# Optimization experiments

Measured on AMD Instinct MI355X. Metric: run time of the kernel, lower is better.

The kernel has to match this reference:

```python
import jax, jax.numpy as jnp
import numpy as np

EMB_DIM = 768
NUM_HEADS = 12
OUT_DIM = 768


def setup_inputs() -> dict:
    key = jax.random.key(0)
    k_x, k_q, k_k, k_v, k_o = jax.random.split(key, 5)
    B, N, D = 8, 1024, EMB_DIM
    s = 1.0 / np.sqrt(D)
    return {
        "x": jax.random.normal(k_x, (B, N, D), dtype=jnp.float32),
        # torch nn.Linear weights are stored [out_features, in_features]
        "Wq": jax.random.normal(k_q, (D, D), dtype=jnp.float32) * s,
        "Wk": jax.random.normal(k_k, (D, D), dtype=jnp.float32) * s,
        "Wv": jax.random.normal(k_v, (D, D), dtype=jnp.float32) * s,
        "Wo": jax.random.normal(k_o, (OUT_DIM, D), dtype=jnp.float32) * s,
    }


def _split_heads(t, H):
    # [B, N, D] -> [B*H, N, D//H]  (heads folded into batch, per einsum 'b i d')
    B, N, D = t.shape
    return t.reshape(B, N, H, D // H).transpose(0, 2, 1, 3).reshape(B * H, N, D // H)


def _merge_heads(t, B, H):
    BH, N, dh = t.shape
    return t.reshape(B, H, N, dh).transpose(0, 2, 1, 3).reshape(B, N, H * dh)


def reference(x, Wq, Wk, Wv, Wo):
    B, N, D = x.shape
    H = NUM_HEADS
    dh = D // H
    # q/k/v projections (torch Linear: y = x @ W.T, no bias)
    q = _split_heads(x @ Wq.T, H)
    k = _split_heads(x @ Wk.T, H)
    v = _split_heads(x @ Wv.T, H)
    scale = dh ** (-0.5)
    # dots: 'b i d , b j d -> b i j' -> full [B*H, N, N] score matrix
    dots = jnp.einsum('bid,bjd->bij', q, k) * scale
    attn = jax.nn.softmax(dots, axis=-1)
    # dropout p=0.0 -> identity
    # vect: 'b i d , b d j -> b i j' == attn @ v
    vect = jnp.einsum('bij,bjd->bid', attn, v)
    out = _merge_heads(vect, B, H) @ Wo.T
    return out
```

## Files before the change

kernel.cpp:

```cpp
#include <hip/hip_runtime.h>
#include <hip/hip_bf16.h>
#include <stdint.h>


typedef __bf16 bf16x8 __attribute__((ext_vector_type(8)));
typedef __bf16 bf16x4 __attribute__((ext_vector_type(4)));
typedef float f32x4 __attribute__((ext_vector_type(4)));

#define GAS __attribute__((address_space(1)))
#define LAS __attribute__((address_space(3)))

__device__ __forceinline__ void glds16(const short* gp, short* lp) {
  __builtin_amdgcn_global_load_lds((const GAS void*)gp, (LAS void*)lp, 16, 0, 0);
}

__device__ __forceinline__ float fast_exp2(float x) {
#if __has_builtin(__builtin_amdgcn_exp2f)
  return __builtin_amdgcn_exp2f(x);
#else
  return __expf(x * 0.6931471805599453f);
#endif
}

__device__ __forceinline__ short bfbits(float f) {
  __bf16 b = (__bf16)f;
  union { __bf16 b; short s; } cv; cv.b = b;
  return cv.s;
}

__device__ __forceinline__ void stage8_f32(const float* __restrict__ src, short* dst) {
  float4 f0 = ((const float4*)src)[0];
  float4 f1 = ((const float4*)src)[1];
  bf16x8 t;
  t[0] = (__bf16)f0.x; t[1] = (__bf16)f0.y; t[2] = (__bf16)f0.z; t[3] = (__bf16)f0.w;
  t[4] = (__bf16)f1.x; t[5] = (__bf16)f1.y; t[6] = (__bf16)f1.z; t[7] = (__bf16)f1.w;
  *(bf16x8*)dst = t;
}

__global__ __launch_bounds__(256) void convert_kernel(
    const float* __restrict__ x, const float* __restrict__ Wq,
    const float* __restrict__ Wk, const float* __restrict__ Wv,
    short* __restrict__ xb, short* __restrict__ wqkv) {
  int seg = blockIdx.y;
  const float* src; short* dst; int n8;
  if (seg == 0) { src = x; dst = xb; n8 = 786432; }
  else {
    src = (seg == 1) ? Wq : (seg == 2) ? Wk : Wv;
    dst = wqkv + (size_t)(seg - 1) * 589824;
    n8 = 73728;
  }
  int idx = blockIdx.x * 256 + threadIdx.x;
  if (idx >= n8) return;
  stage8_f32(src + (size_t)idx * 8, dst + (size_t)idx * 8);
}

__global__ __launch_bounds__(256) void gemm_qkv(
    const short* __restrict__ xb, const short* __restrict__ wqkv,
    short* __restrict__ q, short* __restrict__ k, short* __restrict__ vt) {
  const int m0 = blockIdx.x * 128;
  const int by = blockIdx.y;
  const int n0g = by * 128;
  const int tid = threadIdx.x;
  const int w = tid >> 6, lane = tid & 63, l16 = lane & 15, quad = lane >> 4;
  const int wr = w >> 1, wc = w & 1;

  __shared__ short sA[128 * 64];
  __shared__ short sB[128 * 64];

  f32x4 acc[4][4];
#pragma unroll
  for (int i = 0; i < 4; ++i)
#pragma unroll
    for (int j = 0; j < 4; ++j) acc[i][j] = (f32x4){0.f, 0.f, 0.f, 0.f};

  for (int k0 = 0; k0 < 768; k0 += 64) {
    __syncthreads();
    const short* Ab = xb + (size_t)m0 * 768 + k0;
    const short* Bb = wqkv + (size_t)n0g * 768 + k0;
#pragma unroll
    for (int p = 0; p < 4; ++p) {
      int lin = (w * 4 + p) * 64 + lane;
      int row = lin >> 3;
      int cs = ((lin & 7) ^ (row & 7)) * 8;
      glds16(Ab + (size_t)row * 768 + cs, &sA[lin * 8]);
      glds16(Bb + (size_t)row * 768 + cs, &sB[lin * 8]);
    }
    __syncthreads();
#pragma unroll
    for (int kk2 = 0; kk2 < 2; ++kk2) {
      bf16x8 af[4], bfg[4];
#pragma unroll
      for (int t = 0; t < 4; ++t) {
        int ra = wr * 64 + t * 16 + l16;
        af[t] = *(const bf16x8*)&sA[ra * 64 + (((kk2 * 4 + quad) ^ (ra & 7)) << 3)];
        int rb = wc * 64 + t * 16 + l16;
        bfg[t] = *(const bf16x8*)&sB[rb * 64 + (((kk2 * 4 + quad) ^ (rb & 7)) << 3)];
      }
#pragma unroll
      for (int ti = 0; ti < 4; ++ti)
#pragma unroll
        for (int tj = 0; tj < 4; ++tj)
          acc[ti][tj] = __builtin_amdgcn_mfma_f32_16x16x32_bf16(af[ti], bfg[tj], acc[ti][tj], 0, 0, 0);
    }
  }

  const int wsel = by / 6;
  const int nl0 = (by % 6) * 128 + wc * 64;
  if (wsel == 2) {
#pragma unroll
    for (int ti = 0; ti < 4; ++ti)
#pragma unroll
      for (int tj = 0; tj < 4; ++tj) {
        int token = m0 + wr * 64 + ti * 16 + quad * 4;
        int nl = nl0 + tj * 16 + l16;
        int bh = (token >> 10) * 12 + (nl >> 6);
        short tmp[4];
#pragma unroll
        for (int r = 0; r < 4; ++r) tmp[r] = bfbits(acc[ti][tj][r]);
        *(uint2*)(vt + (size_t)bh * 65536 + (size_t)(nl & 63) * 1024 + (token & 1023)) =
            *(const uint2*)tmp;
      }
  } else {
    short* C = wsel ? k : q;
    const float sc = wsel ? 1.0f : 0.1803368801111244f;
#pragma unroll
    for (int ti = 0; ti < 4; ++ti)
#pragma unroll
      for (int tj = 0; tj < 4; ++tj)
#pragma unroll
        for (int r = 0; r < 4; ++r) {
          int row = m0 + wr * 64 + ti * 16 + quad * 4 + r;
          int nl = nl0 + tj * 16 + l16;
          C[(size_t)row * 768 + nl] = bfbits(acc[ti][tj][r] * sc);
        }
  }
}

__global__ __launch_bounds__(256) void attn_kernel(
    const short* __restrict__ q, const short* __restrict__ k,
    const short* __restrict__ vt, short* __restrict__ vect) {
  const int bh = blockIdx.x % 96;
  const int qt = blockIdx.x / 96;
  const int b = bh / 12, h = bh % 12;
  const int m0 = qt * 128;
  const int tid = threadIdx.x;
  const int w = tid >> 6, lane = tid & 63, l16 = lane & 15, quad = lane >> 4;

  __shared__ short sQ[128 * 64];
  __shared__ short sK[64 * 64];
  __shared__ short sVt[64 * 64];

  const size_t base = (size_t)b * 786432 + (size_t)h * 64;
  const size_t vbase = (size_t)bh * 65536;

#pragma unroll
  for (int p = 0; p < 4; ++p) {
    int lin = (w * 4 + p) * 64 + lane;
    int row = lin >> 3;
    int cs = ((lin & 7) ^ (row & 7)) * 8;
    glds16(q + base + (size_t)(m0 + row) * 768 + cs, &sQ[lin * 8]);
  }
  __syncthreads();
  bf16x8 bq[2][2];
#pragma unroll
  for (int g = 0; g < 2; ++g)
#pragma unroll
    for (int kk = 0; kk < 2; ++kk) {
      int row = w * 32 + g * 16 + l16;
      bq[g][kk] = *(const bf16x8*)&sQ[row * 64 + (((kk * 4 + quad) ^ (row & 7)) << 3)];
    }

  f32x4 l4[2];
  f32x4 oacc[2][4];
#pragma unroll
  for (int g = 0; g < 2; ++g) {
    l4[g] = (f32x4){0.f, 0.f, 0.f, 0.f};
#pragma unroll
    for (int td = 0; td < 4; ++td) oacc[g][td] = (f32x4){0.f, 0.f, 0.f, 0.f};
  }

  for (int j0 = 0; j0 < 1024; j0 += 64) {
    __syncthreads();
#pragma unroll
    for (int p = 0; p < 2; ++p) {
      int lin = (w * 2 + p) * 64 + lane;
      int row = lin >> 3;
      int cs = ((lin & 7) ^ (row & 7)) * 8;
      glds16(k + base + (size_t)(j0 + row) * 768 + cs, &sK[lin * 8]);
      glds16(vt + vbase + (size_t)row * 1024 + j0 + cs, &sVt[lin * 8]);
    }
    __syncthreads();

    f32x4 s[2][4];
#pragma unroll
    for (int g = 0; g < 2; ++g)
#pragma unroll
      for (int ti = 0; ti < 4; ++ti) s[g][ti] = (f32x4){0.f, 0.f, 0.f, 0.f};
#pragma unroll
    for (int kk = 0; kk < 2; ++kk)
#pragma unroll
      for (int ti = 0; ti < 4; ++ti) {
        int row = ti * 16 + l16;
        bf16x8 a = *(const bf16x8*)&sK[row * 64 + (((kk * 4 + quad) ^ (row & 7)) << 3)];
        s[0][ti] = __builtin_amdgcn_mfma_f32_16x16x32_bf16(a, bq[0][kk], s[0][ti], 0, 0, 0);
        s[1][ti] = __builtin_amdgcn_mfma_f32_16x16x32_bf16(a, bq[1][kk], s[1][ti], 0, 0, 0);
      }

    bf16x4 pb[2][4];
#pragma unroll
    for (int g = 0; g < 2; ++g)
#pragma unroll
      for (int ti = 0; ti < 4; ++ti) {
        f32x4 e;
        e[0] = fast_exp2(s[g][ti][0]);
        e[1] = fast_exp2(s[g][ti][1]);
        e[2] = fast_exp2(s[g][ti][2]);
        e[3] = fast_exp2(s[g][ti][3]);
        l4[g] += e;
        bf16x4 t;
        t[0] = (__bf16)e[0]; t[1] = (__bf16)e[1];
        t[2] = (__bf16)e[2]; t[3] = (__bf16)e[3];
        pb[g][ti] = t;
      }

#pragma unroll
    for (int t2 = 0; t2 < 2; ++t2) {
      bf16x8 av[4];
#pragma unroll
      for (int td = 0; td < 4; ++td) {
        int row = td * 16 + l16;
        int o1 = t2 * 32 + quad * 4;
        int c1 = o1 >> 3, w1 = o1 & 7;
        int c2 = c1 + 2;
        union { uint2 u[2]; bf16x8 v; } tmp;
        tmp.u[0] = *(const uint2*)&sVt[row * 64 + ((c1 ^ (row & 7)) << 3) + w1];
        tmp.u[1] = *(const uint2*)&sVt[row * 64 + ((c2 ^ (row & 7)) << 3) + w1];
        av[td] = tmp.v;
      }
#pragma unroll
      for (int g = 0; g < 2; ++g) {
        union { bf16x4 h[2]; bf16x8 v; } bp;
        bp.h[0] = pb[g][2 * t2];
        bp.h[1] = pb[g][2 * t2 + 1];
#pragma unroll
        for (int td = 0; td < 4; ++td)
          oacc[g][td] = __builtin_amdgcn_mfma_f32_16x16x32_bf16(av[td], bp.v, oacc[g][td], 0, 0, 0);
      }
    }
  }

#pragma unroll
  for (int g = 0; g < 2; ++g) {
    float l = (l4[g][0] + l4[g][1]) + (l4[g][2] + l4[g][3]);
    l += __shfl_xor(l, 16);
    l += __shfl_xor(l, 32);
    float inv = 1.0f / l;
    int i_tok = m0 + w * 32 + g * 16 + l16;
#pragma unroll
    for (int td = 0; td < 4; ++td) {
      short tmp[4];
#pragma unroll
      for (int r = 0; r < 4; ++r) tmp[r] = bfbits(oacc[g][td][r] * inv);
      *(uint2*)(vect + base + (size_t)i_tok * 768 + td * 16 + quad * 4) = *(const uint2*)tmp;
    }
  }
}

__global__ __launch_bounds__(256) void gemm_out(
    const short* __restrict__ vect, const float* __restrict__ Wo,
    float* __restrict__ out) {
  const int m0 = blockIdx.x * 128;
  const int n0 = blockIdx.y * 128;
  const int tid = threadIdx.x;
  const int w = tid >> 6, lane = tid & 63, l16 = lane & 15, quad = lane >> 4;
  const int wr = w >> 1, wc = w & 1;

  __shared__ short sA[128 * 64];
  __shared__ short sB[128 * 64];

  f32x4 acc[4][4];
#pragma unroll
  for (int i = 0; i < 4; ++i)
#pragma unroll
    for (int j = 0; j < 4; ++j) acc[i][j] = (f32x4){0.f, 0.f, 0.f, 0.f};

  for (int k0 = 0; k0 < 768; k0 += 64) {
    __syncthreads();
    const short* Ab = vect + (size_t)m0 * 768 + k0;
#pragma unroll
    for (int p = 0; p < 4; ++p) {
      int lin = (w * 4 + p) * 64 + lane;
      int row = lin >> 3;
      int cs = ((lin & 7) ^ (row & 7)) * 8;
      glds16(Ab + (size_t)row * 768 + cs, &sA[lin * 8]);
      stage8_f32(Wo + (size_t)(n0 + row) * 768 + k0 + cs, &sB[lin * 8]);
    }
    __syncthreads();
#pragma unroll
    for (int kk2 = 0; kk2 < 2; ++kk2) {
      bf16x8 af[4], bfg[4];
#pragma unroll
      for (int t = 0; t < 4; ++t) {
        int ra = wr * 64 + t * 16 + l16;
        af[t] = *(const bf16x8*)&sA[ra * 64 + (((kk2 * 4 + quad) ^ (ra & 7)) << 3)];
        int rb = wc * 64 + t * 16 + l16;
        bfg[t] = *(const bf16x8*)&sB[rb * 64 + (((kk2 * 4 + quad) ^ (rb & 7)) << 3)];
      }
#pragma unroll
      for (int ti = 0; ti < 4; ++ti)
#pragma unroll
        for (int tj = 0; tj < 4; ++tj)
          acc[ti][tj] = __builtin_amdgcn_mfma_f32_16x16x32_bf16(af[ti], bfg[tj], acc[ti][tj], 0, 0, 0);
    }
  }
#pragma unroll
  for (int ti = 0; ti < 4; ++ti)
#pragma unroll
    for (int tj = 0; tj < 4; ++tj)
#pragma unroll
      for (int r = 0; r < 4; ++r) {
        int row = m0 + wr * 64 + ti * 16 + quad * 4 + r;
        int col = n0 + wc * 64 + tj * 16 + l16;
        out[(size_t)row * 768 + col] = acc[ti][tj][r];
      }
}

extern "C" void kernel_launch(void* const* d_in, const int* in_sizes, int n_in,
                              void* d_out, int out_size, void* d_ws, size_t ws_size,
                              hipStream_t stream) {
  const float* x  = (const float*)d_in[0];
  const float* Wq = (const float*)d_in[1];
  const float* Wk = (const float*)d_in[2];
  const float* Wv = (const float*)d_in[3];
  const float* Wo = (const float*)d_in[4];
  float* out = (float*)d_out;

  const size_t MN = (size_t)8192 * 768;
  short* q    = (short*)d_ws;
  short* k    = q + MN;
  short* vt   = k + MN;
  short* vect = vt + MN;

  short* xb   = (short*)d_out;
  short* wqkv = xb + MN;

  convert_kernel<<<dim3(3072, 4), 256, 0, stream>>>(x, Wq, Wk, Wv, xb, wqkv);
  gemm_qkv<<<dim3(64, 18), 256, 0, stream>>>(xb, wqkv, q, k, vt);
  attn_kernel<<<768, 256, 0, stream>>>(q, k, vt, vect);
  gemm_out<<<dim3(64, 6), 256, 0, stream>>>(vect, Wo, out);
}
```

Before: 198.8 us.

## Double-buffer attention K/V tiles and pre-convert Wo to bf16 for output GEMM

The attention loop now double-buffers its K and V^T shared-memory tiles. The next tile is fetched asynchronously while the current one is multiplied, and there is one barrier per iteration instead of two. Wo is converted to bf16 once in the convert kernel, so gemm_out can use direct global-to-LDS loads instead of fp32 loads plus per-block conversion. gemm_out also uses 64-row tiles, doubling the block count, and vect reuses the q buffer. The costs are more LDS per attention block, which may lower occupancy, and an aliasing between q and vect that relies on each block reading its Q tile before writing the same region.

Result: no change. 201.1 us (+1.2%).

```diff
diff --git a/kernel.cpp b/kernel.cpp
--- a/kernel.cpp
+++ b/kernel.cpp
@@ -40,10 +40,12 @@
 __global__ __launch_bounds__(256) void convert_kernel(
     const float* __restrict__ x, const float* __restrict__ Wq,
     const float* __restrict__ Wk, const float* __restrict__ Wv,
-    short* __restrict__ xb, short* __restrict__ wqkv) {
+    const float* __restrict__ Wo,
+    short* __restrict__ xb, short* __restrict__ wqkv, short* __restrict__ wob) {
   int seg = blockIdx.y;
   const float* src; short* dst; int n8;
   if (seg == 0) { src = x; dst = xb; n8 = 786432; }
+  else if (seg == 4) { src = Wo; dst = wob; n8 = 73728; }
   else {
     src = (seg == 1) ? Wq : (seg == 2) ? Wk : Wv;
     dst = wqkv + (size_t)(seg - 1) * 589824;
@@ -147,8 +149,8 @@
   const int w = tid >> 6, lane = tid & 63, l16 = lane & 15, quad = lane >> 4;
 
   __shared__ short sQ[128 * 64];
-  __shared__ short sK[64 * 64];
-  __shared__ short sVt[64 * 64];
+  __shared__ short sK[2][64 * 64];
+  __shared__ short sVt[2][64 * 64];
 
   const size_t base = (size_t)b * 786432 + (size_t)h * 64;
   const size_t vbase = (size_t)bh * 65536;
@@ -160,7 +162,16 @@
     int cs = ((lin & 7) ^ (row & 7)) * 8;
     glds16(q + base + (size_t)(m0 + row) * 768 + cs, &sQ[lin * 8]);
   }
+#pragma unroll
+  for (int p = 0; p < 2; ++p) {
+    int lin = (w * 2 + p) * 64 + lane;
+    int row = lin >> 3;
+    int cs = ((lin & 7) ^ (row & 7)) * 8;
+    glds16(k + base + (size_t)row * 768 + cs, &sK[0][lin * 8]);
+    glds16(vt + vbase + (size_t)row * 1024 + cs, &sVt[0][lin * 8]);
+  }
   __syncthreads();
+
   bf16x8 bq[2][2];
 #pragma unroll
   for (int g = 0; g < 2; ++g)
@@ -179,17 +190,22 @@
     for (int td = 0; td < 4; ++td) oacc[g][td] = (f32x4){0.f, 0.f, 0.f, 0.f};
   }
 
-  for (int j0 = 0; j0 < 1024; j0 += 64) {
-    __syncthreads();
-#pragma unroll
-    for (int p = 0; p < 2; ++p) {
-      int lin = (w * 2 + p) * 64 + lane;
-      int row = lin >> 3;
-      int cs = ((lin & 7) ^ (row & 7)) * 8;
-      glds16(k + base + (size_t)(j0 + row) * 768 + cs, &sK[lin * 8]);
-      glds16(vt + vbase + (size_t)row * 1024 + j0 + cs, &sVt[lin * 8]);
-    }
-    __syncthreads();
+  for (int t = 0; t < 16; ++t) {
+    if (t < 15) {
+      int j0n = (t + 1) * 64;
+      short* sKn = sK[(t + 1) & 1];
+      short* sVn = sVt[(t + 1) & 1];
+#pragma unroll
+      for (int p = 0; p < 2; ++p) {
+        int lin = (w * 2 + p) * 64 + lane;
+        int row = lin >> 3;
+        int cs = ((lin & 7) ^ (row & 7)) * 8;
+        glds16(k + base + (size_t)(j0n + row) * 768 + cs, &sKn[lin * 8]);
+        glds16(vt + vbase + (size_t)row * 1024 + j0n + cs, &sVn[lin * 8]);
+      }
+    }
+    const short* sKc = sK[t & 1];
+    const short* sVc = sVt[t & 1];
 
     f32x4 s[2][4];
 #pragma unroll
@@ -201,7 +217,7 @@
 #pragma unroll
       for (int ti = 0; ti < 4; ++ti) {
         int row = ti * 16 + l16;
-        bf16x8 a = *(const bf16x8*)&sK[row * 64 + (((kk * 4 + quad) ^ (row & 7)) << 3)];
+        bf16x8 a = *(const bf16x8*)&sKc[row * 64 + (((kk * 4 + quad) ^ (row & 7)) << 3)];
         s[0][ti] = __builtin_amdgcn_mfma_f32_16x16x32_bf16(a, bq[0][kk], s[0][ti], 0, 0, 0);
         s[1][ti] = __builtin_amdgcn_mfma_f32_16x16x32_bf16(a, bq[1][kk], s[1][ti], 0, 0, 0);
       }
@@ -217,10 +233,10 @@
         e[2] = fast_exp2(s[g][ti][2]);
         e[3] = fast_exp2(s[g][ti][3]);
         l4[g] += e;
-        bf16x4 t;
-        t[0] = (__bf16)e[0]; t[1] = (__bf16)e[1];
-        t[2] = (__bf16)e[2]; t[3] = (__bf16)e[3];
-        pb[g][ti] = t;
+        bf16x4 tb;
+        tb[0] = (__bf16)e[0]; tb[1] = (__bf16)e[1];
+        tb[2] = (__bf16)e[2]; tb[3] = (__bf16)e[3];
+        pb[g][ti] = tb;
       }
 
 #pragma unroll
@@ -233,8 +249,8 @@
         int c1 = o1 >> 3, w1 = o1 & 7;
         int c2 = c1 + 2;
         union { uint2 u[2]; bf16x8 v; } tmp;
-        tmp.u[0] = *(const uint2*)&sVt[row * 64 + ((c1 ^ (row & 7)) << 3) + w1];
-        tmp.u[1] = *(const uint2*)&sVt[row * 64 + ((c2 ^ (row & 7)) << 3) + w1];
+        tmp.u[0] = *(const uint2*)&sVc[row * 64 + ((c1 ^ (row & 7)) << 3) + w1];
+        tmp.u[1] = *(const uint2*)&sVc[row * 64 + ((c2 ^ (row & 7)) << 3) + w1];
         av[td] = tmp.v;
       }
 #pragma unroll
@@ -247,6 +263,7 @@
           oacc[g][td] = __builtin_amdgcn_mfma_f32_16x16x32_bf16(av[td], bp.v, oacc[g][td], 0, 0, 0);
       }
     }
+    if (t < 15) __syncthreads();
   }
 
 #pragma unroll
@@ -267,59 +284,69 @@
 }
 
 __global__ __launch_bounds__(256) void gemm_out(
-    const short* __restrict__ vect, const float* __restrict__ Wo,
+    const short* __restrict__ vect, const short* __restrict__ wob,
     float* __restrict__ out) {
-  const int m0 = blockIdx.x * 128;
+  const int m0 = blockIdx.x * 64;
   const int n0 = blockIdx.y * 128;
   const int tid = threadIdx.x;
   const int w = tid >> 6, lane = tid & 63, l16 = lane & 15, quad = lane >> 4;
   const int wr = w >> 1, wc = w & 1;
 
-  __shared__ short sA[128 * 64];
+  __shared__ short sA[64 * 64];
   __shared__ short sB[128 * 64];
 
-  f32x4 acc[4][4];
-#pragma unroll
-  for (int i = 0; i < 4; ++i)
+  f32x4 acc[2][4];
+#pragma unroll
+  for (int i = 0; i < 2; ++i)
 #pragma unroll
     for (int j = 0; j < 4; ++j) acc[i][j] = (f32x4){0.f, 0.f, 0.f, 0.f};
 
   for (int k0 = 0; k0 < 768; k0 += 64) {
     __syncthreads();
     const short* Ab = vect + (size_t)m0 * 768 + k0;
+    const short* Bb = wob + (size_t)n0 * 768 + k0;
+#pragma unroll
+    for (int p = 0; p < 2; ++p) {
+      int lin = (w * 2 + p) * 64 + lane;
+      int row = lin >> 3;
+      int cs = ((lin & 7) ^ (row & 7)) * 8;
+      glds16(Ab + (size_t)row * 768 + cs, &sA[lin * 8]);
+    }
 #pragma unroll
     for (int p = 0; p < 4; ++p) {
       int lin = (w * 4 + p) * 64 + lane;
       int row = lin >> 3;
       int cs = ((lin & 7) ^ (row & 7)) * 8;
-      glds16(Ab + (size_t)row * 768 + cs, &sA[lin * 8]);
-      stage8_f32(Wo + (size_t)(n0 + row) * 768 + k0 + cs, &sB[lin * 8]);
+      glds16(Bb + (size_t)row * 768 + cs, &sB[lin * 8]);
     }
     __syncthreads();
 #pragma unroll
     for (int kk2 = 0; kk2 < 2; ++kk2) {
-      bf16x8 af[4], bfg[4];
+      bf16x8 af[2], bfg[4];
+#pragma unroll
+      for (int t = 0; t < 2; ++t) {
+        int ra = wr * 32 + t * 16 + l16;
+        af[t] = *(const bf16x8*)&sA[ra * 64 + (((kk2 * 4 + quad) ^ (ra & 7)) << 3)];
+      }
 #pragma unroll
       for (int t = 0; t < 4; ++t) {
-        int ra = wr * 64 + t * 16 + l16;
-        af[t] = *(const bf16x8*)&sA[ra * 64 + (((kk2 * 4 + quad) ^ (ra & 7)) << 3)];
         int rb = wc * 64 + t * 16 + l16;
         bfg[t] = *(const bf16x8*)&sB[rb * 64 + (((kk2 * 4 + quad) ^ (rb & 7)) << 3)];
       }
 #pragma unroll
-      for (int ti = 0; ti < 4; ++ti)
+      for (int ti = 0; ti < 2; ++ti)
 #pragma unroll
         for (int tj = 0; tj < 4; ++tj)
           acc[ti][tj] = __builtin_amdgcn_mfma_f32_16x16x32_bf16(af[ti], bfg[tj], acc[ti][tj], 0, 0, 0);
     }
   }
 #pragma unroll
-  for (int ti = 0; ti < 4; ++ti)
+  for (int ti = 0; ti < 2; ++ti)
 #pragma unroll
     for (int tj = 0; tj < 4; ++tj)
 #pragma unroll
       for (int r = 0; r < 4; ++r) {
-        int row = m0 + wr * 64 + ti * 16 + quad * 4 + r;
+        int row = m0 + wr * 32 + ti * 16 + quad * 4 + r;
         int col = n0 + wc * 64 + tj * 16 + l16;
         out[(size_t)row * 768 + col] = acc[ti][tj][r];
       }
@@ -339,13 +366,14 @@
   short* q    = (short*)d_ws;
   short* k    = q + MN;
   short* vt   = k + MN;
-  short* vect = vt + MN;
+  short* vect = q;
+  short* wob  = vt + MN;
 
   short* xb   = (short*)d_out;
   short* wqkv = xb + MN;
 
-  convert_kernel<<<dim3(3072, 4), 256, 0, stream>>>(x, Wq, Wk, Wv, xb, wqkv);
+  convert_kernel<<<dim3(3072, 5), 256, 0, stream>>>(x, Wq, Wk, Wv, Wo, xb, wqkv, wob);
   gemm_qkv<<<dim3(64, 18), 256, 0, stream>>>(xb, wqkv, q, k, vt);
   attn_kernel<<<768, 256, 0, stream>>>(q, k, vt, vect);
-  gemm_out<<<dim3(64, 6), 256, 0, stream>>>(vect, Wo, out);
-}
+  gemm_out<<<dim3(128, 6), 256, 0, stream>>>(vect, wob, out);
+}
```
